# Optimization experiments

Measured on AMD Instinct MI355X. Metric: run time of the kernel, lower is better.

The kernel has to match this reference:

```python
import jax, jax.numpy as jnp
import numpy as np

B, L, D, H, N_LAYERS = 32, 512, 1024, 1024, 4

def setup_inputs() -> dict:
    key = jax.random.key(0)
    ks = jax.random.split(key, 3)
    x = jax.random.normal(ks[0], (B, L, D), dtype=jnp.float32)
    h0 = jnp.zeros((N_LAYERS, B, H), dtype=jnp.float32)
    # Xavier-normal init: std = sqrt(2/(fan_in+fan_out))
    std = float(np.sqrt(2.0 / (H + H)))
    WI = jax.random.normal(ks[1], (N_LAYERS, H, H), dtype=jnp.float32) * std  # layer 0 uses D==H
    WH = jax.random.normal(ks[2], (N_LAYERS, H, H), dtype=jnp.float32) * std
    BI = jnp.zeros((N_LAYERS, H), dtype=jnp.float32)
    BH = jnp.zeros((N_LAYERS, H), dtype=jnp.float32)
    return {"x": x, "h0": h0, "WI": WI, "BI": BI, "WH": WH, "BH": BH}

def reference(x, h0, WI, BI, WH, BH):
    n_layers = WI.shape[0]

    def step(h_prev, x_t):
        # h_prev: [n_layers, B, H]; x_t: [B, D]
        inp = x_t
        hs = []
        for l in range(n_layers):
            h_new = jnp.tanh(inp @ WI[l].T + BI[l] + h_prev[l] @ WH[l].T + BH[l])
            hs.append(h_new)
            inp = h_new
        h = jnp.stack(hs, axis=0)
        return h, hs[-1]

    xs = jnp.swapaxes(x, 0, 1)  # [L, B, D]
    h_final, out = jax.lax.scan(step, h0, xs)
    output = jnp.swapaxes(out, 0, 1)  # [B, L, H]
    return output, h_final
```

## Files before the change

### kernel.cpp

```cpp
#include <hip/hip_runtime.h>
#include <hip/hip_fp16.h>

#define BB 32
#define LL 512
#define HH 1024
#define NL 4
#define TPL 16
#define CPB 64
#define TAGM 0x0001000100010001ULL
#define SROW 1032

typedef unsigned long long ull;
typedef _Float16 f16x8 __attribute__((ext_vector_type(8)));
typedef float    f32x4 __attribute__((ext_vector_type(4)));

__device__ __forceinline__ f16x8 cvt8(const float* __restrict__ p) {
  f32x4 lo = *reinterpret_cast<const f32x4*>(p);
  f32x4 hi = *reinterpret_cast<const f32x4*>(p + 4);
  f16x8 r;
#pragma unroll
  for (int e = 0; e < 4; ++e) { r[e] = (_Float16)lo[e]; r[e + 4] = (_Float16)hi[e]; }
  return r;
}

__device__ __forceinline__ ull tag_bad(f16x8 v, ull want) {
  union { f16x8 v; ull u[2]; } c; c.v = v;
  return ((c.u[0] ^ want) | (c.u[1] ^ want)) & TAGM;
}

__device__ __forceinline__ f16x8 fix_q(const _Float16* __restrict__ gsrc, ull want) {
  const ull* p = reinterpret_cast<const ull*>(gsrc);
  union { ull u[2]; f16x8 v; } c;
  do {
    c.u[0] = __hip_atomic_load(p, __ATOMIC_RELAXED, __HIP_MEMORY_SCOPE_AGENT);
  } while ((c.u[0] ^ want) & TAGM);
  do {
    c.u[1] = __hip_atomic_load(p + 1, __ATOMIC_RELAXED, __HIP_MEMORY_SCOPE_AGENT);
  } while ((c.u[1] ^ want) & TAGM);
  return c.v;
}

__global__ __launch_bounds__(512, 2) void rnn_persist(
    const float* __restrict__ x,
    const float* __restrict__ h0,
    const float* __restrict__ WI,
    const float* __restrict__ BI,
    const float* __restrict__ WH,
    const float* __restrict__ BH,
    float* __restrict__ out,
    _Float16* __restrict__ hbuf,
    unsigned* __restrict__ pflag,
    int rsmask, int rshift) {
  const int l = blockIdx.x & 7;
  if (l >= NL) return;
  const int tile = blockIdx.x >> 3;
  const int c0   = tile * CPB;
  const int tid  = threadIdx.x;
  const int w    = tid >> 6;
  const int lane = tid & 63;
  const int crow = lane & 15;
  const int kgrp = lane >> 4;

  extern __shared__ char smem[];
  _Float16* sIn  = (_Float16*)smem;
  _Float16* sHid = sIn + 32 * SROW;
  float*    redp = (float*)smem;
#define RED(W2, R, C) redp[(((W2) * 32 + (R)) * 68) + (C)]

  f16x8 wIf[4][4], wHf[4][4];
  {
    const float* WIb = WI + (size_t)l * HH * HH;
    const float* WHb = WH + (size_t)l * HH * HH;
#pragma unroll
    for (int ct = 0; ct < 4; ++ct) {
      const size_t row = (size_t)(c0 + ct * 16 + crow) * HH;
#pragma unroll
      for (int j = 0; j < 4; ++j) {
        const int k = w * 128 + kgrp * 8 + j * 32;
        wIf[ct][j] = cvt8(WIb + row + k);
        wHf[ct][j] = cvt8(WHb + row + k);
      }
    }
  }

  const int rb = tid >> 4;
  const int c4 = (tid & 15) * 4;
  float bias4[4];
#pragma unroll
  for (int j = 0; j < 4; ++j)
    bias4[j] = BI[l * HH + c0 + c4 + j] + BH[l * HH + c0 + c4 + j];

  for (int t = 0; t < LL; ++t) {
    const ull wantI = (((t >> rshift) & 1) ^ 1) ? TAGM : 0ULL;
    const ull wantH = ((((t - 1) >> rshift) & 1) ^ 1) ? TAGM : 0ULL;

    if (tid < 48) {
      if (tid < 16) {
        if (l > 0)
          while (__hip_atomic_load(&pflag[(l - 1) * TPL + tid], __ATOMIC_RELAXED,
                                   __HIP_MEMORY_SCOPE_AGENT) < (unsigned)(t + 1))
            __builtin_amdgcn_s_sleep(1);
      } else if (tid >= 32) {
        const int Lt = tid - 32;
        if (l < NL - 1 && t > rsmask)
          while (__hip_atomic_load(&pflag[(l + 1) * TPL + Lt], __ATOMIC_RELAXED,
                                   __HIP_MEMORY_SCOPE_AGENT) < (unsigned)(t - rsmask))
            __builtin_amdgcn_s_sleep(1);
      }
    }
    __syncthreads();

    if (tid == 0 && t > 0)
      __hip_atomic_store(&pflag[l * TPL + tile], (unsigned)t, __ATOMIC_RELAXED,
                         __HIP_MEMORY_SCOPE_AGENT);

    const _Float16* srcI =
        hbuf + ((size_t)(l - 1) * (rsmask + 1) + (t & rsmask)) * BB * HH;
    const _Float16* srcH =
        hbuf + ((size_t)l * (rsmask + 1) + ((t - 1) & rsmask)) * BB * HH;

    {
      f16x8 tq[8];
      if (l == 0) {
#pragma unroll
        for (int it = 0; it < 8; ++it) {
          const int q = it * 512 + tid, row = q >> 7, col = (q & 127) * 8;
          tq[it] = cvt8(x + ((size_t)row * LL + t) * HH + col);
        }
      } else {
#pragma unroll
        for (int it = 0; it < 8; ++it) {
          const int q = it * 512 + tid, row = q >> 7, col = (q & 127) * 8;
          tq[it] = *reinterpret_cast<const f16x8*>(srcI + (size_t)row * HH + col);
        }
        ull badI = 0;
#pragma unroll
        for (int it = 0; it < 8; ++it) badI |= tag_bad(tq[it], wantI);
        if (badI) {
#pragma unroll
          for (int it = 0; it < 8; ++it) {
            const int q = it * 512 + tid, row = q >> 7, col = (q & 127) * 8;
            if (tag_bad(tq[it], wantI))
              tq[it] = fix_q(srcI + (size_t)row * HH + col, wantI);
          }
        }
      }
#pragma unroll
      for (int it = 0; it < 8; ++it) {
        const int q = it * 512 + tid, row = q >> 7, col = (q & 127) * 8;
        *reinterpret_cast<f16x8*>(&sIn[(size_t)row * SROW + col]) = tq[it];
      }
    }

    {
      f16x8 tq[8];
      if (t == 0) {
#pragma unroll
        for (int it = 0; it < 8; ++it) {
          const int q = it * 512 + tid, row = q >> 7, col = (q & 127) * 8;
          tq[it] = cvt8(h0 + ((size_t)l * BB + row) * HH + col);
        }
      } else {
#pragma unroll
        for (int it = 0; it < 8; ++it) {
          const int q = it * 512 + tid, row = q >> 7, col = (q & 127) * 8;
          tq[it] = *reinterpret_cast<const f16x8*>(srcH + (size_t)row * HH + col);
        }
        ull badH = 0;
#pragma unroll
        for (int it = 0; it < 8; ++it) badH |= tag_bad(tq[it], wantH);
        if (badH) {
#pragma unroll
          for (int it = 0; it < 8; ++it) {
            const int q = it * 512 + tid, row = q >> 7, col = (q & 127) * 8;
            const _Float16* a = srcH + (size_t)row * HH + col;
            int tries = 0;
            while (tag_bad(tq[it], wantH)) {
              if (tries++ < 64) {
                const volatile ull* vp = reinterpret_cast<const volatile ull*>(a);
                ull lo = vp[0], hi = vp[1];
                union { ull u[2]; f16x8 v; } c; c.u[0] = lo; c.u[1] = hi;
                tq[it] = c.v;
              } else {
                tq[it] = fix_q(a, wantH);
              }
            }
          }
        }
      }
#pragma unroll
      for (int it = 0; it < 8; ++it) {
        const int q = it * 512 + tid, row = q >> 7, col = (q & 127) * 8;
        *reinterpret_cast<f16x8*>(&sHid[(size_t)row * SROW + col]) = tq[it];
      }
    }
    __syncthreads();

    f32x4 acc[4][2];
#pragma unroll
    for (int ct = 0; ct < 4; ++ct)
#pragma unroll
      for (int rt = 0; rt < 2; ++rt) acc[ct][rt] = (f32x4){0.f, 0.f, 0.f, 0.f};
#pragma unroll
    for (int j = 0; j < 4; ++j) {
      const int base = w * 128 + kgrp * 8 + j * 32;
      f16x8 ai0 = *reinterpret_cast<const f16x8*>(&sIn [(size_t)crow * SROW + base]);
      f16x8 ai1 = *reinterpret_cast<const f16x8*>(&sIn [(size_t)(16 + crow) * SROW + base]);
      f16x8 ah0 = *reinterpret_cast<const f16x8*>(&sHid[(size_t)crow * SROW + base]);
      f16x8 ah1 = *reinterpret_cast<const f16x8*>(&sHid[(size_t)(16 + crow) * SROW + base]);
#pragma unroll
      for (int ct = 0; ct < 4; ++ct) {
        acc[ct][0] = __builtin_amdgcn_mfma_f32_16x16x32_f16(ai0, wIf[ct][j], acc[ct][0], 0, 0, 0);
        acc[ct][1] = __builtin_amdgcn_mfma_f32_16x16x32_f16(ai1, wIf[ct][j], acc[ct][1], 0, 0, 0);
        acc[ct][0] = __builtin_amdgcn_mfma_f32_16x16x32_f16(ah0, wHf[ct][j], acc[ct][0], 0, 0, 0);
        acc[ct][1] = __builtin_amdgcn_mfma_f32_16x16x32_f16(ah1, wHf[ct][j], acc[ct][1], 0, 0, 0);
      }
    }
    __syncthreads();

#pragma unroll
    for (int ct = 0; ct < 4; ++ct)
#pragma unroll
      for (int rt = 0; rt < 2; ++rt)
#pragma unroll
        for (int r = 0; r < 4; ++r)
          RED(w, rt * 16 + kgrp * 4 + r, ct * 16 + crow) = acc[ct][rt][r];
    __syncthreads();

    float v[4];
#pragma unroll
    for (int j = 0; j < 4; ++j) {
      float s = bias4[j];
#pragma unroll
      for (int w2 = 0; w2 < 8; ++w2) s += RED(w2, rb, c4 + j);
      v[j] = tanhf(s);
    }
    {
      union { _Float16 h[4]; ull u; } pk;
#pragma unroll
      for (int j = 0; j < 4; ++j) pk.h[j] = (_Float16)v[j];
      const ull tg = (((t >> rshift) & 1) ^ 1) ? TAGM : 0ULL;
      pk.u = (pk.u & ~TAGM) | tg;
      const size_t off =
          ((size_t)l * (rsmask + 1) + (t & rsmask)) * BB * HH + (size_t)rb * HH + c0 + c4;
      *reinterpret_cast<ull*>(hbuf + off) = pk.u;
      __hip_atomic_store(reinterpret_cast<ull*>(hbuf + off), pk.u,
                         __ATOMIC_RELAXED, __HIP_MEMORY_SCOPE_AGENT);
    }
    if (l == NL - 1) {
      f32x4 o = {v[0], v[1], v[2], v[3]};
      __builtin_nontemporal_store(
          o, reinterpret_cast<f32x4*>(out + ((size_t)rb * LL + t) * HH + c0 + c4));
    }
    if (t == LL - 1) {
      f32x4 o = {v[0], v[1], v[2], v[3]};
      __builtin_nontemporal_store(
          o, reinterpret_cast<f32x4*>(out + (size_t)BB * LL * HH +
                                      ((size_t)l * BB + rb) * HH + c0 + c4));
    }
  }

  __syncthreads();
  if (tid == 0)
    __hip_atomic_store(&pflag[l * TPL + tile], (unsigned)LL, __ATOMIC_RELAXED,
                       __HIP_MEMORY_SCOPE_AGENT);
#undef RED
}

extern "C" void kernel_launch(void* const* d_in, const int* in_sizes, int n_in,
                              void* d_out, int out_size, void* d_ws, size_t ws_size,
                              hipStream_t stream) {
  const float* x  = (const float*)d_in[0];
  const float* h0 = (const float*)d_in[1];
  const float* WI = (const float*)d_in[2];
  const float* BI = (const float*)d_in[3];
  const float* WH = (const float*)d_in[4];
  const float* BH = (const float*)d_in[5];
  float* out = (float*)d_out;

  const size_t perSlot = (size_t)NL * BB * HH * sizeof(_Float16);
  int rs = 512;
  while (rs > 8 && (size_t)rs * perSlot + 65536 > ws_size) rs >>= 1;
  int rshift = 0;
  while ((1 << rshift) < rs) ++rshift;

  _Float16* hbuf = (_Float16*)d_ws;
  unsigned* pflag = (unsigned*)((char*)d_ws + (size_t)rs * perSlot);

  const int smemBytes = 2 * 32 * SROW * (int)sizeof(_Float16);
  static int attrSet = 0;
  if (!attrSet) {
    hipFuncSetAttribute(reinterpret_cast<const void*>(rnn_persist),
                        hipFuncAttributeMaxDynamicSharedMemorySize, smemBytes);
    attrSet = 1;
  }

  hipMemsetAsync(pflag, 0, (size_t)NL * TPL * sizeof(unsigned), stream);
  rnn_persist<<<128, 512, smemBytes, stream>>>(x, h0, WI, BI, WH, BH, out, hbuf,
                                               pflag, rs - 1, rshift);
}
```

Measured before the change: 3.535 ms.

## Use 1024-thread blocks covering 128 columns with 2-way K split

Each persistent block now owns 128 output columns using 16 waves, arranged as 8 column groups by 2 K halves, in place of 64 columns over 8 K-split waves. Half as many blocks take part per layer, which halves the cross-block flag polling and the number of blocks re-staging the full input and hidden state into LDS each step. The cross-wave reduction shrinks from 8 partials to 2. The cost is that only 32 blocks do work, so fewer CUs are active, and each thread now holds 32 weight fragments in registers.

```diff
diff --git a/kernel.cpp b/kernel.cpp
--- a/kernel.cpp
+++ b/kernel.cpp
@@ -5,8 +5,8 @@
 #define LL 512
 #define HH 1024
 #define NL 4
-#define TPL 16
-#define CPB 64
+#define TPL 8
+#define CPB 128
 #define TAGM 0x0001000100010001ULL
 #define SROW 1032
 
@@ -40,7 +40,7 @@
   return c.v;
 }
 
-__global__ __launch_bounds__(512, 2) void rnn_persist(
+__global__ __launch_bounds__(1024, 1) void rnn_persist(
     const float* __restrict__ x,
     const float* __restrict__ h0,
     const float* __restrict__ WI,
@@ -57,6 +57,8 @@
   const int c0   = tile * CPB;
   const int tid  = threadIdx.x;
   const int w    = tid >> 6;
+  const int kw   = w >> 3;
+  const int cg   = w & 7;
   const int lane = tid & 63;
   const int crow = lane & 15;
   const int kgrp = lane >> 4;
@@ -65,26 +67,23 @@
   _Float16* sIn  = (_Float16*)smem;
   _Float16* sHid = sIn + 32 * SROW;
   float*    redp = (float*)smem;
-#define RED(W2, R, C) redp[(((W2) * 32 + (R)) * 68) + (C)]
-
-  f16x8 wIf[4][4], wHf[4][4];
+#define RED(KW, R, C) redp[(((KW) * 32 + (R)) * 132) + (C)]
+
+  f16x8 wIf[16], wHf[16];
   {
     const float* WIb = WI + (size_t)l * HH * HH;
     const float* WHb = WH + (size_t)l * HH * HH;
-#pragma unroll
-    for (int ct = 0; ct < 4; ++ct) {
-      const size_t row = (size_t)(c0 + ct * 16 + crow) * HH;
-#pragma unroll
-      for (int j = 0; j < 4; ++j) {
-        const int k = w * 128 + kgrp * 8 + j * 32;
-        wIf[ct][j] = cvt8(WIb + row + k);
-        wHf[ct][j] = cvt8(WHb + row + k);
-      }
+    const size_t row = (size_t)(c0 + cg * 16 + crow) * HH;
+#pragma unroll
+    for (int j = 0; j < 16; ++j) {
+      const int k = kw * 512 + j * 32 + kgrp * 8;
+      wIf[j] = cvt8(WIb + row + k);
+      wHf[j] = cvt8(WHb + row + k);
     }
   }
 
-  const int rb = tid >> 4;
-  const int c4 = (tid & 15) * 4;
+  const int rb = tid >> 5;
+  const int c4 = (tid & 31) * 4;
   float bias4[4];
 #pragma unroll
   for (int j = 0; j < 4; ++j)
@@ -95,12 +94,12 @@
     const ull wantH = ((((t - 1) >> rshift) & 1) ^ 1) ? TAGM : 0ULL;
 
     if (tid < 48) {
-      if (tid < 16) {
+      if (tid < 8) {
         if (l > 0)
           while (__hip_atomic_load(&pflag[(l - 1) * TPL + tid], __ATOMIC_RELAXED,
                                    __HIP_MEMORY_SCOPE_AGENT) < (unsigned)(t + 1))
             __builtin_amdgcn_s_sleep(1);
-      } else if (tid >= 32) {
+      } else if (tid >= 32 && tid < 40) {
         const int Lt = tid - 32;
         if (l < NL - 1 && t > rsmask)
           while (__hip_atomic_load(&pflag[(l + 1) * TPL + Lt], __ATOMIC_RELAXED,
@@ -120,59 +119,59 @@
         hbuf + ((size_t)l * (rsmask + 1) + ((t - 1) & rsmask)) * BB * HH;
 
     {
-      f16x8 tq[8];
+      f16x8 tq[4];
       if (l == 0) {
 #pragma unroll
-        for (int it = 0; it < 8; ++it) {
-          const int q = it * 512 + tid, row = q >> 7, col = (q & 127) * 8;
+        for (int it = 0; it < 4; ++it) {
+          const int q = it * 1024 + tid, row = q >> 7, col = (q & 127) * 8;
           tq[it] = cvt8(x + ((size_t)row * LL + t) * HH + col);
         }
       } else {
 #pragma unroll
-        for (int it = 0; it < 8; ++it) {
-          const int q = it * 512 + tid, row = q >> 7, col = (q & 127) * 8;
+        for (int it = 0; it < 4; ++it) {
+          const int q = it * 1024 + tid, row = q >> 7, col = (q & 127) * 8;
           tq[it] = *reinterpret_cast<const f16x8*>(srcI + (size_t)row * HH + col);
         }
         ull badI = 0;
 #pragma unroll
-        for (int it = 0; it < 8; ++it) badI |= tag_bad(tq[it], wantI);
+        for (int it = 0; it < 4; ++it) badI |= tag_bad(tq[it], wantI);
         if (badI) {
 #pragma unroll
-          for (int it = 0; it < 8; ++it) {
-            const int q = it * 512 + tid, row = q >> 7, col = (q & 127) * 8;
+          for (int it = 0; it < 4; ++it) {
+            const int q = it * 1024 + tid, row = q >> 7, col = (q & 127) * 8;
             if (tag_bad(tq[it], wantI))
               tq[it] = fix_q(srcI + (size_t)row * HH + col, wantI);
           }
         }
       }
 #pragma unroll
-      for (int it = 0; it < 8; ++it) {
-        const int q = it * 512 + tid, row = q >> 7, col = (q & 127) * 8;
+      for (int it = 0; it < 4; ++it) {
+        const int q = it * 1024 + tid, row = q >> 7, col = (q & 127) * 8;
         *reinterpret_cast<f16x8*>(&sIn[(size_t)row * SROW + col]) = tq[it];
       }
     }
 
     {
-      f16x8 tq[8];
+      f16x8 tq[4];
       if (t == 0) {
 #pragma unroll
-        for (int it = 0; it < 8; ++it) {
-          const int q = it * 512 + tid, row = q >> 7, col = (q & 127) * 8;
+        for (int it = 0; it < 4; ++it) {
+          const int q = it * 1024 + tid, row = q >> 7, col = (q & 127) * 8;
           tq[it] = cvt8(h0 + ((size_t)l * BB + row) * HH + col);
         }
       } else {
 #pragma unroll
-        for (int it = 0; it < 8; ++it) {
-          const int q = it * 512 + tid, row = q >> 7, col = (q & 127) * 8;
+        for (int it = 0; it < 4; ++it) {
+          const int q = it * 1024 + tid, row = q >> 7, col = (q & 127) * 8;
           tq[it] = *reinterpret_cast<const f16x8*>(srcH + (size_t)row * HH + col);
         }
         ull badH = 0;
 #pragma unroll
-        for (int it = 0; it < 8; ++it) badH |= tag_bad(tq[it], wantH);
+        for (int it = 0; it < 4; ++it) badH |= tag_bad(tq[it], wantH);
         if (badH) {
 #pragma unroll
-          for (int it = 0; it < 8; ++it) {
-            const int q = it * 512 + tid, row = q >> 7, col = (q & 127) * 8;
+          for (int it = 0; it < 4; ++it) {
+            const int q = it * 1024 + tid, row = q >> 7, col = (q & 127) * 8;
             const _Float16* a = srcH + (size_t)row * HH + col;
             int tries = 0;
             while (tag_bad(tq[it], wantH)) {
@@ -189,52 +188,41 @@
         }
       }
 #pragma unroll
-      for (int it = 0; it < 8; ++it) {
-        const int q = it * 512 + tid, row = q >> 7, col = (q & 127) * 8;
+      for (int it = 0; it < 4; ++it) {
+        const int q = it * 1024 + tid, row = q >> 7, col = (q & 127) * 8;
         *reinterpret_cast<f16x8*>(&sHid[(size_t)row * SROW + col]) = tq[it];
       }
     }
     __syncthreads();
 
-    f32x4 acc[4][2];
-#pragma unroll
-    for (int ct = 0; ct < 4; ++ct)
-#pragma unroll
-      for (int rt = 0; rt < 2; ++rt) acc[ct][rt] = (f32x4){0.f, 0.f, 0.f, 0.f};
-#pragma unroll
-    for (int j = 0; j < 4; ++j) {
-      const int base = w * 128 + kgrp * 8 + j * 32;
+    f32x4 acc[2];
+    acc[0] = (f32x4){0.f, 0.f, 0.f, 0.f};
+    acc[1] = (f32x4){0.f, 0.f, 0.f, 0.f};
+#pragma unroll
+    for (int j = 0; j < 16; ++j) {
+      const int base = kw * 512 + j * 32 + kgrp * 8;
       f16x8 ai0 = *reinterpret_cast<const f16x8*>(&sIn [(size_t)crow * SROW + base]);
       f16x8 ai1 = *reinterpret_cast<const f16x8*>(&sIn [(size_t)(16 + crow) * SROW + base]);
       f16x8 ah0 = *reinterpret_cast<const f16x8*>(&sHid[(size_t)crow * SROW + base]);
       f16x8 ah1 = *reinterpret_cast<const f16x8*>(&sHid[(size_t)(16 + crow) * SROW + base]);
-#pragma unroll
-      for (int ct = 0; ct < 4; ++ct) {
-        acc[ct][0] = __builtin_amdgcn_mfma_f32_16x16x32_f16(ai0, wIf[ct][j], acc[ct][0], 0, 0, 0);
-        acc[ct][1] = __builtin_amdgcn_mfma_f32_16x16x32_f16(ai1, wIf[ct][j], acc[ct][1], 0, 0, 0);
-        acc[ct][0] = __builtin_amdgcn_mfma_f32_16x16x32_f16(ah0, wHf[ct][j], acc[ct][0], 0, 0, 0);
-        acc[ct][1] = __builtin_amdgcn_mfma_f32_16x16x32_f16(ah1, wHf[ct][j], acc[ct][1], 0, 0, 0);
-      }
-    }
-    __syncthreads();
-
-#pragma unroll
-    for (int ct = 0; ct < 4; ++ct)
-#pragma unroll
-      for (int rt = 0; rt < 2; ++rt)
-#pragma unroll
-        for (int r = 0; r < 4; ++r)
-          RED(w, rt * 16 + kgrp * 4 + r, ct * 16 + crow) = acc[ct][rt][r];
+      acc[0] = __builtin_amdgcn_mfma_f32_16x16x32_f16(ai0, wIf[j], acc[0], 0, 0, 0);
+      acc[1] = __builtin_amdgcn_mfma_f32_16x16x32_f16(ai1, wIf[j], acc[1], 0, 0, 0);
+      acc[0] = __builtin_amdgcn_mfma_f32_16x16x32_f16(ah0, wHf[j], acc[0], 0, 0, 0);
+      acc[1] = __builtin_amdgcn_mfma_f32_16x16x32_f16(ah1, wHf[j], acc[1], 0, 0, 0);
+    }
+    __syncthreads();
+
+#pragma unroll
+    for (int rt = 0; rt < 2; ++rt)
+#pragma unroll
+      for (int r = 0; r < 4; ++r)
+        RED(kw, rt * 16 + kgrp * 4 + r, cg * 16 + crow) = acc[rt][r];
     __syncthreads();
 
     float v[4];
 #pragma unroll
-    for (int j = 0; j < 4; ++j) {
-      float s = bias4[j];
-#pragma unroll
-      for (int w2 = 0; w2 < 8; ++w2) s += RED(w2, rb, c4 + j);
-      v[j] = tanhf(s);
-    }
+    for (int j = 0; j < 4; ++j)
+      v[j] = tanhf(bias4[j] + RED(0, rb, c4 + j) + RED(1, rb, c4 + j));
     {
       union { _Float16 h[4]; ull u; } pk;
 #pragma unroll
@@ -296,6 +284,6 @@
   }
 
   hipMemsetAsync(pflag, 0, (size_t)NL * TPL * sizeof(unsigned), stream);
-  rnn_persist<<<128, 512, smemBytes, stream>>>(x, h0, WI, BI, WH, BH, out, hbuf,
+  rnn_persist<<<64, 1024, smemBytes, stream>>>(x, h0, WI, BI, WH, BH, out, hbuf,
                                                pflag, rs - 1, rshift);
 }
```

After: 10.07 ms. 185% more time.
